# Optimization experiments

Measured on AMD Instinct MI355X. Metric: run time of the kernel, lower is better.

The kernel has to match this reference:

```python
import jax, jax.numpy as jnp
import numpy as np

D = 128        # embed_dims
P = 4          # num_points
G = 1          # num_groups
L = 4          # num_levels
NC = 6         # cameras
HB, WB = 200, 200
QN = HB * WB
NUM_LAYERS = 2
IMG_H, IMG_W = 256, 704
EPS = 1e-5
PC_MIN = np.array([-50.0, -50.0, -5.0], np.float32)
PC_EXT = np.array([100.0, 100.0, 8.0], np.float32)
LEVEL_HW = [(32, 88), (16, 44), (8, 22), (4, 11)]


def layer_norm(x, g, b):
    m = x.mean(-1, keepdims=True)
    v = jnp.mean((x - m) ** 2, axis=-1, keepdims=True)
    return (x - m) * jax.lax.rsqrt(v + 1e-5) * g + b


def bilinear(feat, u, v):
    # feat: (B,H,W,C); u,v: (B,N) normalized to [0,1]; zero padding, align_corners=False
    B, H, W, C = feat.shape
    x = u * W - 0.5
    y = v * H - 0.5
    x0f = jnp.floor(x)
    y0f = jnp.floor(y)
    wx = (x - x0f)[..., None]
    wy = (y - y0f)[..., None]
    x0 = x0f.astype(jnp.int32)
    y0 = y0f.astype(jnp.int32)
    bi = jnp.arange(B)[:, None]

    def gather(xi, yi):
        valid = ((xi >= 0) & (xi < W) & (yi >= 0) & (yi < H)).astype(feat.dtype)[..., None]
        return feat[bi, jnp.clip(yi, 0, H - 1), jnp.clip(xi, 0, W - 1)] * valid

    return (gather(x0, y0) * (1 - wx) * (1 - wy)
            + gather(x0 + 1, y0) * wx * (1 - wy)
            + gather(x0, y0 + 1) * (1 - wx) * wy
            + gather(x0 + 1, y0 + 1) * wx * wy)


def cam_contrib(l2i_n, hom, sw, cam_feats):
    # l2i_n: (B,4,4); hom: (B,Q,G,P,4); sw: (B,Q,G,P,L); cam_feats: L x (B,Hl,Wl,C)
    p2 = jnp.einsum('bij,bqgpj->bqgpi', l2i_n, hom)
    z = p2[..., 2]
    zc = jnp.maximum(z, EPS)
    u = p2[..., 0] / (zc * IMG_W)
    v = p2[..., 1] / (zc * IMG_H)
    mask = (z > EPS) & (u >= 0) & (u <= 1) & (v >= 0) & (v <= 1)
    B = hom.shape[0]
    uf = u.reshape(B, -1)
    vf = v.reshape(B, -1)
    out = jnp.zeros(hom.shape[:4] + (cam_feats[0].shape[-1],), cam_feats[0].dtype)
    for l in range(L):
        s = bilinear(cam_feats[l], uf, vf).reshape(B, -1, G, P, cam_feats[l].shape[-1])
        out = out + s * sw[..., l:l + 1]
    return out * mask[..., None].astype(out.dtype)


def forward(feat0, feat1, feat2, feat3, lidar2img, bev_query, bev_pos,
            pe_w1, pe_b1, pe_w2, pe_b2, conv1_w, conv1_b, conv2_w, conv2_b,
            off_w, off_b, sw_w, sw_b, cp_w1, cp_b1, cp_w2, cp_b2, cp_w3, cp_b3,
            ffn_w1, ffn_b1, ffn_w2, ffn_b2, n1_g, n1_b, n2_g, n2_b, n3_g, n3_b):
    # (b,n,C,h,w) -> (b,n,h,w,C), matching the decoder's rearrange (g=1)
    feats = [jnp.transpose(f, (0, 1, 3, 4, 2)) for f in (feat0, feat1, feat2, feat3)]
    B = bev_query.shape[0]
    pc_min = jnp.asarray(PC_MIN)
    pc_ext = jnp.asarray(PC_EXT)
    # position embedding of bev_pos is identical every layer
    pos_embed = jax.nn.relu(bev_pos @ pe_w1 + pe_b1) @ pe_w2 + pe_b2
    q = bev_query
    for _ in range(NUM_LAYERS):
        # in_conv: 1x1 conv + GELU + 5x5 conv on 200x200 BEV grid
        qe = (q + pos_embed).reshape(B, HB, WB, D)
        h = jax.nn.gelu(qe @ conv1_w + conv1_b, approximate=False)
        h = jax.lax.conv_general_dilated(h, conv2_w, (1, 1), 'SAME',
                                         dimension_numbers=('NHWC', 'HWIO', 'NHWC')) + conv2_b
        q = q + h.reshape(B, QN, D)
        q = layer_norm(q, n1_g, n1_b)
        # DetSegSampling
        off = (q @ off_w + off_b).reshape(B, QN, G, P, 3)
        ref = bev_pos[:, :, None, None, :] * pc_ext + pc_min
        pts = ref + off
        sw = jax.nn.softmax((q @ sw_w + sw_b).reshape(B, QN, G, P, L), axis=-1)
        hom = jnp.concatenate([pts, jnp.ones_like(pts[..., :1])], -1)
        acc = jnp.zeros((B, QN, G, P, D), q.dtype)
        for n in range(NC):
            acc = acc + cam_contrib(lidar2img[:, n], hom, sw,
                                    tuple(f[:, n] for f in feats))
        # 'b q g p c -> b q (p g c)' then 3-layer compressor MLP (1x1 convs)
        flat = jnp.transpose(acc, (0, 1, 3, 2, 4)).reshape(B, QN, P * G * D)
        h = jax.nn.relu(flat @ cp_w1 + cp_b1)
        h = jax.nn.relu(h @ cp_w2 + cp_b2)
        h = h @ cp_w3 + cp_b3
        q = q + h
        q = layer_norm(q, n2_g, n2_b)
        q = q + (jax.nn.relu(q @ ffn_w1 + ffn_b1) @ ffn_w2 + ffn_b2)
        q = layer_norm(q, n3_g, n3_b)
    return q


def _make_lidar2img():
    fx = fy = 500.0
    K = np.array([[fx, 0, IMG_W / 2, 0], [0, fy, IMG_H / 2, 0],
                  [0, 0, 1, 0], [0, 0, 0, 1]], np.float32)
    mats = []
    for n in range(NC):
        yaw = 2 * np.pi * n / NC
        c, s = np.cos(yaw), np.sin(yaw)
        # camera n looks along (cos yaw, sin yaw, 0), mounted 1.5m above lidar
        E = np.array([[s, -c, 0, 0], [0, 0, -1, 1.5], [c, s, 0, 0], [0, 0, 0, 1]], np.float32)
        mats.append(K @ E)
    return jnp.asarray(np.stack(mats))[None]  # (1,NC,4,4)


def setup_inputs() -> dict:
    key = jax.random.key(0)
    ks = jax.random.split(key, 24)
    sc = 0.02
    inp = {}
    for i, (h, w) in enumerate(LEVEL_HW):
        inp[f'feat{i}'] = jax.random.normal(ks[i], (1, NC, D, h, w), jnp.float32)
    inp['lidar2img'] = _make_lidar2img()
    inp['bev_query'] = jax.random.normal(ks[4], (1, QN, D), jnp.float32)
    inp['bev_pos'] = jax.random.uniform(ks[5], (1, QN, 3), jnp.float32)
    inp['pe_w1'] = jax.random.normal(ks[6], (3, 2 * D), jnp.float32) * sc
    inp['pe_b1'] = jnp.zeros((2 * D,), jnp.float32)
    inp['pe_w2'] = jax.random.normal(ks[7], (2 * D, D), jnp.float32) * sc
    inp['pe_b2'] = jnp.zeros((D,), jnp.float32)
    inp['conv1_w'] = jax.random.normal(ks[8], (D, D), jnp.float32) * sc
    inp['conv1_b'] = jnp.zeros((D,), jnp.float32)
    inp['conv2_w'] = jax.random.normal(ks[9], (5, 5, D, D), jnp.float32) * sc
    inp['conv2_b'] = jnp.zeros((D,), jnp.float32)
    inp['off_w'] = jax.random.normal(ks[10], (D, G * P * 3), jnp.float32) * 0.01
    inp['off_b'] = jax.random.uniform(ks[11], (G * P * 3,), jnp.float32, -0.5, 0.5)
    inp['sw_w'] = jax.random.normal(ks[12], (D, G * P * L), jnp.float32) * sc
    inp['sw_b'] = jnp.zeros((G * P * L,), jnp.float32)
    inp['cp_w1'] = jax.random.normal(ks[13], (P * G * D, 4 * D), jnp.float32) * sc
    inp['cp_b1'] = jnp.zeros((4 * D,), jnp.float32)
    inp['cp_w2'] = jax.random.normal(ks[14], (4 * D, 4 * D), jnp.float32) * sc
    inp['cp_b2'] = jnp.zeros((4 * D,), jnp.float32)
    inp['cp_w3'] = jax.random.normal(ks[15], (4 * D, D), jnp.float32) * sc
    inp['cp_b3'] = jnp.zeros((D,), jnp.float32)
    inp['ffn_w1'] = jax.random.normal(ks[16], (D, D), jnp.float32) * sc
    inp['ffn_b1'] = jnp.zeros((D,), jnp.float32)
    inp['ffn_w2'] = jax.random.normal(ks[17], (D, D), jnp.float32) * sc
    inp['ffn_b2'] = jnp.zeros((D,), jnp.float32)
    for i in (1, 2, 3):
        inp[f'n{i}_g'] = jnp.ones((D,), jnp.float32)
        inp[f'n{i}_b'] = jnp.zeros((D,), jnp.float32)
    return inp


def reference(feat0, feat1, feat2, feat3, lidar2img, bev_query, bev_pos,
              pe_w1, pe_b1, pe_w2, pe_b2, conv1_w, conv1_b, conv2_w, conv2_b,
              off_w, off_b, sw_w, sw_b, cp_w1, cp_b1, cp_w2, cp_b2, cp_w3, cp_b3,
              ffn_w1, ffn_b1, ffn_w2, ffn_b2, n1_g, n1_b, n2_g, n2_b, n3_g, n3_b):
    return forward(feat0, feat1, feat2, feat3, lidar2img, bev_query, bev_pos,
                   pe_w1, pe_b1, pe_w2, pe_b2, conv1_w, conv1_b, conv2_w, conv2_b,
                   off_w, off_b, sw_w, sw_b, cp_w1, cp_b1, cp_w2, cp_b2, cp_w3, cp_b3,
                   ffn_w1, ffn_b1, ffn_w2, ffn_b2, n1_g, n1_b, n2_g, n2_b, n3_g, n3_b)
```

## Files before the change

kernel.cpp:

```cpp
#include <hip/hip_runtime.h>
#include <hip/hip_bf16.h>

typedef unsigned short u16;
typedef unsigned char u8;
typedef __attribute__((ext_vector_type(8))) short bf16x8;
typedef __attribute__((ext_vector_type(4))) float f32x4;
typedef __attribute__((ext_vector_type(2))) float f32x2;

#define DEV __device__ __forceinline__

DEV float b2f(u16 s){ return __uint_as_float(((unsigned)s) << 16); }
DEV u16 f2b(float f){
    unsigned u = __float_as_uint(f);
    u = u + 0x7fffu + ((u >> 16) & 1u);
    return (u16)(u >> 16);
}
DEV u8 f2f8(float v){
    int r = __builtin_amdgcn_cvt_pk_fp8_f32(v, v, 0, false);
    return (u8)(r & 0xff);
}
DEV unsigned f2f8x4(float a, float b, float c, float d){
    int lo = __builtin_amdgcn_cvt_pk_fp8_f32(a, b, 0, false);
    int r  = __builtin_amdgcn_cvt_pk_fp8_f32(c, d, lo, true);
    return (unsigned)r;
}
DEV void storeElem(float* p, float v){ *p = v; }
DEV void storeElem(u16* p, float v){ *p = f2b(v); }
DEV void storeElem(u8* p, float v){ *p = f2f8(v); }

template<int ACT> DEV float actf(float x){
    if (ACT == 1) return fmaxf(x, 0.f);
    if (ACT == 2) return 0.5f * x * (1.f + erff(x * 0.70710678118654752f));
    return x;
}

DEV void gload16(const void* g, void* l){
    __builtin_amdgcn_global_load_lds(
        (const __attribute__((address_space(1))) void*)g,
        (__attribute__((address_space(3))) void*)l, 16, 0, 0);
}

__global__ void transpose_feat(const float* __restrict__ in, u8* __restrict__ out,
                               int H, int W){
    int total = 6 * H * W * 32;
    int lin = blockIdx.x * 256 + threadIdx.x;
    if (lin >= total) return;
    int c4   = (lin & 31) * 4;
    int pix  = lin >> 5;
    int x    = pix % W;
    int rest = pix / W;
    int y    = rest % H;
    int n    = rest / H;
    int HW   = H * W;
    size_t ib = ((size_t)(n * 128 + c4) * H + y) * W + x;
    unsigned v4 = f2f8x4(in[ib], in[ib + (size_t)HW],
                         in[ib + (size_t)2 * HW], in[ib + (size_t)3 * HW]);
    *(unsigned*)&out[(size_t)pix * 128 + c4] = v4;
}

__global__ void prep_wt(const float* __restrict__ w, u16* __restrict__ o, int K, int N){
    int id = blockIdx.x * 256 + threadIdx.x;
    if (id >= K * N) return;
    int n = id / K, k = id % K;
    o[id] = f2b(w[(size_t)k * N + n]);
}
__global__ void prep_wt_f8(const float* __restrict__ w, u8* __restrict__ o, int K, int N){
    int id = blockIdx.x * 256 + threadIdx.x;
    if (id >= K * N) return;
    int n = id / K, k = id % K;
    o[id] = f2f8(w[(size_t)k * N + n]);
}
__global__ void prep_cvt16(const float* __restrict__ src, u16* __restrict__ dst, int n4){
    int i4 = blockIdx.x * 256 + threadIdx.x;
    if (i4 >= n4) return;
    float4 a = *(const float4*)&src[(size_t)i4 * 4];
    ushort4 v; v.x = f2b(a.x); v.y = f2b(a.y); v.z = f2b(a.z); v.w = f2b(a.w);
    *(ushort4*)&dst[(size_t)i4 * 4] = v;
}
__global__ void prep_osw_w(const float* __restrict__ off_w, const float* __restrict__ off_b,
                           const float* __restrict__ sw_w, const float* __restrict__ sw_b,
                           u16* __restrict__ owsT, float* __restrict__ obias){
    int id = blockIdx.x * 256 + threadIdx.x;
    if (id >= 4096) return;
    int n = id >> 7, k = id & 127;
    float w = (n < 12) ? off_w[k * 12 + n] : (n < 28) ? sw_w[k * 16 + (n - 12)] : 0.f;
    owsT[n * 128 + k] = f2b(w);
    if (k == 0) obias[n] = (n < 12) ? off_b[n] : (n < 28) ? sw_b[n - 12] : 0.f;
}
__global__ void prep_conv_w_f8(const float* __restrict__ w, u8* __restrict__ o){
    int id = blockIdx.x * 256 + threadIdx.x;
    if (id >= 51200) return;
    int slot = id & 15;
    int oc   = (id >> 4) & 127;
    int tap  = id >> 11;
    int ks = slot >> 2, kg = slot & 3;
    int ic0 = ks * 32 + kg * 8;
    u8 tmp[8];
#pragma unroll
    for (int j = 0; j < 8; j++)
        tmp[j] = f2f8(w[((size_t)tap * 128 + ic0 + j) * 128 + oc]);
    *(long*)&o[(size_t)tap * 16384 + ks * 4096 + kg * 1024 + oc * 8] = *(long*)tmp;
}
__global__ void prep_hid(const float* __restrict__ bev_pos,
                         const float* __restrict__ w1, const float* __restrict__ b1,
                         u16* __restrict__ hid){
    int id = blockIdx.x * 256 + threadIdx.x;
    if (id >= 2560000) return;
    int qi = id >> 6, c4 = (id & 63) * 4;
    float p0 = bev_pos[qi * 3 + 0];
    float p1 = bev_pos[qi * 3 + 1];
    float p2 = bev_pos[qi * 3 + 2];
    ushort4 v;
    u16* vp = (u16*)&v;
#pragma unroll
    for (int j = 0; j < 4; j++){
        int ch = c4 + j;
        float h = p0 * w1[ch] + p1 * w1[256 + ch] + p2 * w1[512 + ch] + b1[ch];
        vp[j] = f2b(fmaxf(h, 0.f));
    }
    *(ushort4*)&hid[(size_t)qi * 256 + c4] = v;
}

DEV void stage64(const u16* __restrict__ g, int ldk, u16* lds, int wv, int lane){
    const u16* gp = g + (size_t)(lane >> 3) * ldk + (lane & 7) * 8;
#pragma unroll
    for (int j = 0; j < 4; j++){
        int ch = wv + j * 4;
        gload16(gp + (size_t)ch * 8 * ldk, lds + ch * 512);
    }
}
DEV void stage64f8(const u8* __restrict__ g, int ldk, u8* lds, int wv, int lane){
    int rloc = lane >> 2;
#pragma unroll
    for (int j = 0; j < 2; j++){
        int ch = wv + j * 4;
        int row = ch * 16 + rloc;
        int sp  = (lane & 3) ^ ((row >> 1) & 3);
        gload16(g + (size_t)row * ldk + sp * 16, lds + ch * 1024);
    }
}

template<int K, int ACT, typename TOUT, int NBY = 0, int NBX = 0>
__global__ __launch_bounds__(256) void mfma_gemm(
    const u16* __restrict__ A, const u16* __restrict__ BT,
    const float* __restrict__ bias, TOUT* __restrict__ C, int Ntot){
    __shared__ u16 As[2][128 * 64];
    __shared__ u16 Bs[2][128 * 64];
    const int t = threadIdx.x, wv = t >> 6, lane = t & 63;
    int bx, by;
    if (NBY > 0){
        const int gpx = (NBX + 7) / 8;
        int xcd = blockIdx.x & 7, slot = blockIdx.x >> 3;
        bx = xcd * gpx + slot / NBY;
        by = slot % NBY;
        if (bx >= NBX) return;
    } else { bx = blockIdx.x; by = blockIdx.y; }
    const int r0 = bx * 128, n0 = by * 128;
    const int l15 = lane & 15, kg = lane >> 4;
    const int wr = (wv >> 1) * 64, wc = (wv & 1) * 64;
    f32x4 acc[4][4];
#pragma unroll
    for (int r = 0; r < 4; r++)
#pragma unroll
        for (int c = 0; c < 4; c++) acc[r][c] = (f32x4){0.f, 0.f, 0.f, 0.f};

    stage64(A + (size_t)r0 * K, K, As[0], wv, lane);
    stage64(BT + (size_t)n0 * K, K, Bs[0], wv, lane);
    __syncthreads();
    int buf = 0;
    for (int kc = 0; kc < K / 64; kc++){
        if (kc + 1 < K / 64){
            stage64(A + (size_t)r0 * K + (kc + 1) * 64, K, As[buf ^ 1], wv, lane);
            stage64(BT + (size_t)n0 * K + (kc + 1) * 64, K, Bs[buf ^ 1], wv, lane);
        }
#pragma unroll
        for (int ks = 0; ks < 2; ks++){
            bf16x8 af[4], bfr[4];
#pragma unroll
            for (int r = 0; r < 4; r++)
                af[r] = *(const bf16x8*)&As[buf][(wr + r * 16 + l15) * 64 + ks * 32 + kg * 8];
#pragma unroll
            for (int c = 0; c < 4; c++)
                bfr[c] = *(const bf16x8*)&Bs[buf][(wc + c * 16 + l15) * 64 + ks * 32 + kg * 8];
#pragma unroll
            for (int r = 0; r < 4; r++)
#pragma unroll
                for (int c = 0; c < 4; c++)
                    acc[r][c] = __builtin_amdgcn_mfma_f32_16x16x32_bf16(af[r], bfr[c], acc[r][c], 0, 0, 0);
        }
        __syncthreads();
        buf ^= 1;
    }
#pragma unroll
    for (int c = 0; c < 4; c++){
        int gcol = n0 + wc + c * 16 + l15;
        float bb = bias[gcol];
#pragma unroll
        for (int r = 0; r < 4; r++){
#pragma unroll
            for (int reg = 0; reg < 4; reg++){
                int grow = r0 + wr + r * 16 + kg * 4 + reg;
                storeElem(C + (size_t)grow * Ntot + gcol, actf<ACT>(acc[r][c][reg] + bb));
            }
        }
    }
}

template<int K, int ACT, typename TOUT, int NBY = 0, int NBX = 0>
__global__ __launch_bounds__(256) void mfma_gemm_f8(
    const u8* __restrict__ A, const u8* __restrict__ BT,
    const float* __restrict__ bias, TOUT* __restrict__ C, int Ntot){
    __shared__ __align__(16) u8 As[2][128 * 64];
    __shared__ __align__(16) u8 Bs[2][128 * 64];
    const int t = threadIdx.x, wv = t >> 6, lane = t & 63;
    int bx, by;
    if (NBY > 0){
        const int gpx = (NBX + 7) / 8;
        int xcd = blockIdx.x & 7, slot = blockIdx.x >> 3;
        bx = xcd * gpx + slot / NBY;
        by = slot % NBY;
        if (bx >= NBX) return;
    } else { bx = blockIdx.x; by = blockIdx.y; }
    const int r0 = bx * 128, n0 = by * 128;
    const int l15 = lane & 15, kg = lane >> 4;
    const int wr = (wv >> 1) * 64, wc = (wv & 1) * 64;
    f32x4 acc[4][4];
#pragma unroll
    for (int r = 0; r < 4; r++)
#pragma unroll
        for (int c = 0; c < 4; c++) acc[r][c] = (f32x4){0.f, 0.f, 0.f, 0.f};

    stage64f8(A + (size_t)r0 * K, K, As[0], wv, lane);
    stage64f8(BT + (size_t)n0 * K, K, Bs[0], wv, lane);
    __syncthreads();
    int buf = 0;
    for (int kc = 0; kc < K / 64; kc++){
        if (kc + 1 < K / 64){
            stage64f8(A + (size_t)r0 * K + (kc + 1) * 64, K, As[buf ^ 1], wv, lane);
            stage64f8(BT + (size_t)n0 * K + (kc + 1) * 64, K, Bs[buf ^ 1], wv, lane);
        }
#pragma unroll
        for (int ks = 0; ks < 2; ks++){
            long af[4], bfr[4];
#pragma unroll
            for (int r = 0; r < 4; r++){
                int row = wr + r * 16 + l15;
                int s8 = (ks * 4 + kg) ^ (row & 6);
                af[r] = *(const long*)&As[buf][row * 64 + s8 * 8];
            }
#pragma unroll
            for (int c = 0; c < 4; c++){
                int row = wc + c * 16 + l15;
                int s8 = (ks * 4 + kg) ^ (row & 6);
                bfr[c] = *(const long*)&Bs[buf][row * 64 + s8 * 8];
            }
#pragma unroll
            for (int r = 0; r < 4; r++)
#pragma unroll
                for (int c = 0; c < 4; c++)
                    acc[r][c] = __builtin_amdgcn_mfma_f32_16x16x32_fp8_fp8(af[r], bfr[c], acc[r][c], 0, 0, 0);
        }
        __syncthreads();
        buf ^= 1;
    }
#pragma unroll
    for (int c = 0; c < 4; c++){
        int gcol = n0 + wc + c * 16 + l15;
        float bb = bias[gcol];
#pragma unroll
        for (int r = 0; r < 4; r++){
#pragma unroll
            for (int reg = 0; reg < 4; reg++){
                int grow = r0 + wr + r * 16 + kg * 4 + reg;
                storeElem(C + (size_t)grow * Ntot + gcol, actf<ACT>(acc[r][c][reg] + bb));
            }
        }
    }
}

__global__ __launch_bounds__(256) void mfma_pos(
    const u16* __restrict__ A, const u16* __restrict__ BT,
    const float* __restrict__ bias, const float* __restrict__ bq,
    float* __restrict__ pos, u16* __restrict__ qp16){
    const int K = 256;
    __shared__ u16 As[2][128 * 64];
    __shared__ u16 Bs[2][128 * 64];
    const int t = threadIdx.x, wv = t >> 6, lane = t & 63;
    const int r0 = blockIdx.x * 128;
    const int l15 = lane & 15, kg = lane >> 4;
    const int wr = (wv >> 1) * 64, wc = (wv & 1) * 64;
    f32x4 acc[4][4];
#pragma unroll
    for (int r = 0; r < 4; r++)
#pragma unroll
        for (int c = 0; c < 4; c++) acc[r][c] = (f32x4){0.f, 0.f, 0.f, 0.f};

    stage64(A + (size_t)r0 * K, K, As[0], wv, lane);
    stage64(BT, K, Bs[0], wv, lane);
    __syncthreads();
    int buf = 0;
    for (int kc = 0; kc < 4; kc++){
        if (kc + 1 < 4){
            stage64(A + (size_t)r0 * K + (kc + 1) * 64, K, As[buf ^ 1], wv, lane);
            stage64(BT + (kc + 1) * 64, K, Bs[buf ^ 1], wv, lane);
        }
#pragma unroll
        for (int ks = 0; ks < 2; ks++){
            bf16x8 af[4], bfr[4];
#pragma unroll
            for (int r = 0; r < 4; r++)
                af[r] = *(const bf16x8*)&As[buf][(wr + r * 16 + l15) * 64 + ks * 32 + kg * 8];
#pragma unroll
            for (int c = 0; c < 4; c++)
                bfr[c] = *(const bf16x8*)&Bs[buf][(wc + c * 16 + l15) * 64 + ks * 32 + kg * 8];
#pragma unroll
            for (int r = 0; r < 4; r++)
#pragma unroll
                for (int c = 0; c < 4; c++)
                    acc[r][c] = __builtin_amdgcn_mfma_f32_16x16x32_bf16(af[r], bfr[c], acc[r][c], 0, 0, 0);
        }
        __syncthreads();
        buf ^= 1;
    }
#pragma unroll
    for (int c = 0; c < 4; c++){
        int gcol = wc + c * 16 + l15;
        float bb = bias[gcol];
#pragma unroll
        for (int r = 0; r < 4; r++){
#pragma unroll
            for (int reg = 0; reg < 4; reg++){
                int grow = r0 + wr + r * 16 + kg * 4 + reg;
                int growc = min(grow, 39999);
                float v = acc[r][c][reg] + bb;
                pos[(size_t)grow * 128 + gcol]  = v;
                qp16[(size_t)grow * 128 + gcol] = f2b(v + bq[(size_t)growc * 128 + gcol]);
            }
        }
    }
}

template<int AUXM>
__global__ __launch_bounds__(256) void mfma_ffn_ln(
    const u16* __restrict__ A, const u16* __restrict__ W1T,
    const float* __restrict__ b1, const u16* __restrict__ W2T,
    const float* __restrict__ b2, const u16* __restrict__ qin16,
    const float* __restrict__ gam, const float* __restrict__ bet,
    float* __restrict__ outf, u16* __restrict__ q16out, u16* __restrict__ auxpos,
    const float* __restrict__ pos, int Mlim){
    __shared__ u16 As[2][128 * 64];
    __shared__ u16 Bs[2][128 * 64];
    const int t = threadIdx.x, wv = t >> 6, lane = t & 63;
    const int r0 = blockIdx.x * 128;
    const int l15 = lane & 15, kg = lane >> 4;
    const int wr = wv * 32;
    f32x4 acc[2][8];
#pragma unroll
    for (int r = 0; r < 2; r++)
#pragma unroll
        for (int c = 0; c < 8; c++) acc[r][c] = (f32x4){0.f, 0.f, 0.f, 0.f};

    stage64(A + (size_t)r0 * 128, 128, As[0], wv, lane);
    stage64(A + (size_t)r0 * 128 + 64, 128, As[1], wv, lane);
    stage64(W1T, 128, Bs[0], wv, lane);
    stage64(W1T + 64, 128, Bs[1], wv, lane);
    __syncthreads();
#pragma unroll
    for (int kc = 0; kc < 2; kc++){
#pragma unroll
        for (int ks = 0; ks < 2; ks++){
            bf16x8 af[2], bfr[8];
#pragma unroll
            for (int r = 0; r < 2; r++)
                af[r] = *(const bf16x8*)&As[kc][(wr + r * 16 + l15) * 64 + ks * 32 + kg * 8];
#pragma unroll
            for (int c = 0; c < 8; c++)
                bfr[c] = *(const bf16x8*)&Bs[kc][(c * 16 + l15) * 64 + ks * 32 + kg * 8];
#pragma unroll
            for (int r = 0; r < 2; r++)
#pragma unroll
                for (int c = 0; c < 8; c++)
                    acc[r][c] = __builtin_amdgcn_mfma_f32_16x16x32_bf16(af[r], bfr[c], acc[r][c], 0, 0, 0);
        }
    }
    __syncthreads();
    stage64(W2T, 128, Bs[0], wv, lane);
    stage64(W2T + 64, 128, Bs[1], wv, lane);
#pragma unroll
    for (int c = 0; c < 8; c++){
        int col = c * 16 + l15;
        float bb1 = b1[col];
#pragma unroll
        for (int r = 0; r < 2; r++)
#pragma unroll
            for (int reg = 0; reg < 4; reg++){
                int rowl = wr + r * 16 + kg * 4 + reg;
                As[col >> 6][rowl * 64 + (col & 63)] = f2b(fmaxf(acc[r][c][reg] + bb1, 0.f));
            }
    }
    __syncthreads();
#pragma unroll
    for (int r = 0; r < 2; r++)
#pragma unroll
        for (int c = 0; c < 8; c++) acc[r][c] = (f32x4){0.f, 0.f, 0.f, 0.f};
#pragma unroll
    for (int kc = 0; kc < 2; kc++){
#pragma unroll
        for (int ks = 0; ks < 2; ks++){
            bf16x8 af[2], bfr[8];
#pragma unroll
            for (int r = 0; r < 2; r++)
                af[r] = *(const bf16x8*)&As[kc][(wr + r * 16 + l15) * 64 + ks * 32 + kg * 8];
#pragma unroll
            for (int c = 0; c < 8; c++)
                bfr[c] = *(const bf16x8*)&Bs[kc][(c * 16 + l15) * 64 + ks * 32 + kg * 8];
#pragma unroll
            for (int r = 0; r < 2; r++)
#pragma unroll
                for (int c = 0; c < 8; c++)
                    acc[r][c] = __builtin_amdgcn_mfma_f32_16x16x32_bf16(af[r], bfr[c], acc[r][c], 0, 0, 0);
        }
    }
    float bb[8], gg[8], be[8];
#pragma unroll
    for (int c = 0; c < 8; c++){
        int col = c * 16 + l15;
        bb[c] = b2[col]; gg[c] = gam[col]; be[c] = bet[col];
    }
#pragma unroll
    for (int r = 0; r < 2; r++){
#pragma unroll
        for (int reg = 0; reg < 4; reg++){
            int grow = r0 + wr + r * 16 + kg * 4 + reg;
            const u16* qrow = qin16 + (size_t)grow * 128;
            float s = 0.f, q2 = 0.f;
#pragma unroll
            for (int c = 0; c < 8; c++){
                float x = acc[r][c][reg] + bb[c] + b2f(qrow[c * 16 + l15]);
                acc[r][c][reg] = x;
                s += x; q2 += x * x;
            }
#pragma unroll
            for (int m = 8; m >= 1; m >>= 1){
                s  += __shfl_xor(s, m, 64);
                q2 += __shfl_xor(q2, m, 64);
            }
            float mean = s * 0.0078125f;
            float var  = q2 * 0.0078125f - mean * mean;
            float rs   = rsqrtf(var + 1e-5f);
            bool wr_ok = grow < Mlim;
#pragma unroll
            for (int c = 0; c < 8; c++){
                float o = (acc[r][c][reg] - mean) * rs * gg[c] + be[c];
                int col = c * 16 + l15;
                if (wr_ok){
                    if (AUXM == 0){
                        outf[(size_t)grow * 128 + col] = o;
                    } else {
                        q16out[(size_t)grow * 128 + col] = f2b(o);
                        auxpos[(size_t)grow * 128 + col] = f2b(o + pos[(size_t)grow * 128 + col]);
                    }
                }
            }
        }
    }
}

template<int K>
__global__ __launch_bounds__(256) void mfma_gemm_ln_f8(
    const u8* __restrict__ A, const u8* __restrict__ BT,
    const float* __restrict__ bias, const u16* __restrict__ qin16,
    const float* __restrict__ gam, const float* __restrict__ bet,
    u16* __restrict__ q16out, int Mlim){
    __shared__ __align__(16) u8 As[2][128 * 64];
    __shared__ __align__(16) u8 Bs[2][128 * 64];
    const int t = threadIdx.x, wv = t >> 6, lane = t & 63;
    const int r0 = blockIdx.x * 128;
    const int l15 = lane & 15, kg = lane >> 4;
    const int wr = wv * 32;
    f32x4 acc[2][8];
#pragma unroll
    for (int r = 0; r < 2; r++)
#pragma unroll
        for (int c = 0; c < 8; c++) acc[r][c] = (f32x4){0.f, 0.f, 0.f, 0.f};

    stage64f8(A + (size_t)r0 * K, K, As[0], wv, lane);
    stage64f8(BT, K, Bs[0], wv, lane);
    __syncthreads();
    int buf = 0;
    for (int kc = 0; kc < K / 64; kc++){
        if (kc + 1 < K / 64){
            stage64f8(A + (size_t)r0 * K + (kc + 1) * 64, K, As[buf ^ 1], wv, lane);
            stage64f8(BT + (kc + 1) * 64, K, Bs[buf ^ 1], wv, lane);
        }
#pragma unroll
        for (int ks = 0; ks < 2; ks++){
            long af[2], bfr[8];
#pragma unroll
            for (int r = 0; r < 2; r++){
                int row = wr + r * 16 + l15;
                int s8 = (ks * 4 + kg) ^ (row & 6);
                af[r] = *(const long*)&As[buf][row * 64 + s8 * 8];
            }
#pragma unroll
            for (int c = 0; c < 8; c++){
                int row = c * 16 + l15;
                int s8 = (ks * 4 + kg) ^ (row & 6);
                bfr[c] = *(const long*)&Bs[buf][row * 64 + s8 * 8];
            }
#pragma unroll
            for (int r = 0; r < 2; r++)
#pragma unroll
                for (int c = 0; c < 8; c++)
                    acc[r][c] = __builtin_amdgcn_mfma_f32_16x16x32_fp8_fp8(af[r], bfr[c], acc[r][c], 0, 0, 0);
        }
        __syncthreads();
        buf ^= 1;
    }
    float bb[8], gg[8], be[8];
#pragma unroll
    for (int c = 0; c < 8; c++){
        int col = c * 16 + l15;
        bb[c] = bias[col]; gg[c] = gam[col]; be[c] = bet[col];
    }
#pragma unroll
    for (int r = 0; r < 2; r++){
#pragma unroll
        for (int reg = 0; reg < 4; reg++){
            int grow = r0 + wr + r * 16 + kg * 4 + reg;
            const u16* qrow = qin16 + (size_t)grow * 128;
            float s = 0.f, q2 = 0.f;
#pragma unroll
            for (int c = 0; c < 8; c++){
                float x = acc[r][c][reg] + bb[c] + b2f(qrow[c * 16 + l15]);
                acc[r][c][reg] = x;
                s += x; q2 += x * x;
            }
#pragma unroll
            for (int m = 8; m >= 1; m >>= 1){
                s  += __shfl_xor(s, m, 64);
                q2 += __shfl_xor(q2, m, 64);
            }
            float mean = s * 0.0078125f;
            float var  = q2 * 0.0078125f - mean * mean;
            float rs   = rsqrtf(var + 1e-5f);
            bool wr_ok = grow < Mlim;
#pragma unroll
            for (int c = 0; c < 8; c++){
                float o = (acc[r][c][reg] - mean) * rs * gg[c] + be[c];
                if (wr_ok) q16out[(size_t)grow * 128 + c * 16 + l15] = f2b(o);
            }
        }
    }
}

__global__ __launch_bounds__(256) void mfma_osw(
    const u16* __restrict__ A, const u16* __restrict__ BT,
    const float* __restrict__ bias, float* __restrict__ osw){
    __shared__ u16 As[2][128 * 64];
    __shared__ u16 Bs[2][32 * 64];
    const int t = threadIdx.x, wv = t >> 6, lane = t & 63;
    const int r0 = blockIdx.x * 128;
    const int l15 = lane & 15, kg = lane >> 4;
#pragma unroll
    for (int it = 0; it < 8; it++){
        int id = it * 256 + t;
        int row = id >> 4, slot = id & 15;
        uint4 v = *(const uint4*)&A[(size_t)(r0 + row) * 128 + slot * 8];
        *(uint4*)&As[slot >> 3][row * 64 + (slot & 7) * 8] = v;
    }
#pragma unroll
    for (int it = 0; it < 2; it++){
        int id = it * 256 + t;
        if (id < 512){
            int row = id >> 4, slot = id & 15;
            uint4 v = *(const uint4*)&BT[(size_t)row * 128 + slot * 8];
            *(uint4*)&Bs[slot >> 3][row * 64 + (slot & 7) * 8] = v;
        }
    }
    __syncthreads();
    f32x4 acc[2][2];
#pragma unroll
    for (int r = 0; r < 2; r++)
#pragma unroll
        for (int c = 0; c < 2; c++) acc[r][c] = (f32x4){0.f, 0.f, 0.f, 0.f};
#pragma unroll
    for (int ks = 0; ks < 4; ks++){
        int h = ks >> 1, koff = (ks & 1) * 32 + kg * 8;
        bf16x8 af[2], bfr[2];
#pragma unroll
        for (int r = 0; r < 2; r++)
            af[r] = *(const bf16x8*)&As[h][(wv * 32 + r * 16 + l15) * 64 + koff];
#pragma unroll
        for (int c = 0; c < 2; c++)
            bfr[c] = *(const bf16x8*)&Bs[h][(c * 16 + l15) * 64 + koff];
#pragma unroll
        for (int r = 0; r < 2; r++)
#pragma unroll
            for (int c = 0; c < 2; c++)
                acc[r][c] = __builtin_amdgcn_mfma_f32_16x16x32_bf16(af[r], bfr[c], acc[r][c], 0, 0, 0);
    }
#pragma unroll
    for (int c = 0; c < 2; c++){
        int gcol = c * 16 + l15;
        float bb = bias[gcol];
#pragma unroll
        for (int r = 0; r < 2; r++)
#pragma unroll
            for (int reg = 0; reg < 4; reg++){
                int grow = r0 + wv * 32 + r * 16 + kg * 4 + reg;
                osw[(size_t)grow * 32 + gcol] = acc[r][c][reg] + bb;
            }
    }
}

__global__ __launch_bounds__(256) void proj_kernel(
    const float* __restrict__ osw, const float* __restrict__ bev_pos,
    const float* __restrict__ l2i, uint4* __restrict__ ent4, int* __restrict__ cntb){
    int id = blockIdx.x * 256 + threadIdx.x;
    int qi = id >> 2, p = id & 3;
    const float* row = osw + (size_t)qi * 32;
    float px = bev_pos[qi * 3 + 0] * 100.f - 50.f + row[p * 3 + 0];
    float py = bev_pos[qi * 3 + 1] * 100.f - 50.f + row[p * 3 + 1];
    float pz = bev_pos[qi * 3 + 2] * 8.f   - 5.f  + row[p * 3 + 2];
    float lg[4];
#pragma unroll
    for (int l = 0; l < 4; l++) lg[l] = row[12 + p * 4 + l];
    float mx = fmaxf(fmaxf(lg[0], lg[1]), fmaxf(lg[2], lg[3]));
    float den = 0.f, sw[4];
#pragma unroll
    for (int l = 0; l < 4; l++){ sw[l] = expf(lg[l] - mx); den += sw[l]; }
    float inv = 1.f / den;
#pragma unroll
    for (int l = 0; l < 4; l++) sw[l] *= inv;

    const int HS[4] = {32, 16, 8, 4};
    const int WS[4] = {88, 44, 22, 11};
    const unsigned LOFF[4] = {0u, 2162688u, 2703360u, 2838528u};
    int cnt = 0;
    for (int cam = 0; cam < 6; cam++){
        const float* M = l2i + cam * 16;
        float t0 = M[0] * px + M[1] * py + M[2]  * pz + M[3];
        float t1 = M[4] * px + M[5] * py + M[6]  * pz + M[7];
        float z  = M[8] * px + M[9] * py + M[10] * pz + M[11];
        float zc = fmaxf(z, 1e-5f);
        float u = t0 / (zc * 704.f);
        float v = t1 / (zc * 256.f);
        if (!((z > 1e-5f) && u >= 0.f && u <= 1.f && v >= 0.f && v <= 1.f)) continue;
#pragma unroll
        for (int l = 0; l < 4; l++){
            const int Hl = HS[l], Wl = WS[l];
            float xx = u * (float)Wl - 0.5f;
            float yy = v * (float)Hl - 0.5f;
            float xf = floorf(xx), yf = floorf(yy);
            float wx = xx - xf, wy = yy - yf;
            int ix = (int)xf, iy = (int)yf;
            float sl = sw[l];
            float wx0 = (ix >= 0)      ? 1.f - wx : 0.f;
            float wx1 = (ix < Wl - 1)  ? wx       : 0.f;
            float wy0 = (iy >= 0)      ? 1.f - wy : 0.f;
            float wy1 = (iy < Hl - 1)  ? wy       : 0.f;
            int x0c = max(ix, 0), x1c = min(ix + 1, Wl - 1);
            int y0c = max(iy, 0), y1c = min(iy + 1, Hl - 1);
            unsigned base = LOFF[l] + (unsigned)cam * (unsigned)(Hl * Wl * 128)
                          + (unsigned)(y0c * Wl + x0c) * 128u;
            unsigned dxdy = (unsigned)((x1c - x0c) * 128)
                          | ((unsigned)((y1c - y0c) * Wl * 128) << 16);
            if (cnt < 8){
                uint4 e4;
                e4.x = (unsigned)f2b(sl * wx0 * wy0) | ((unsigned)f2b(sl * wx1 * wy0) << 16);
                e4.y = (unsigned)f2b(sl * wx0 * wy1) | ((unsigned)f2b(sl * wx1 * wy1) << 16);
                e4.z = base;
                e4.w = dxdy;
                ent4[(size_t)cnt * 160000 + id] = e4;
                cnt++;
            }
        }
    }
    cntb[id] = cnt;
}

DEV void fma8f8(float* acc, uint2 v, float w){
    f32x2 p0 = __builtin_amdgcn_cvt_pk_f32_fp8(v.x, false);
    f32x2 p1 = __builtin_amdgcn_cvt_pk_f32_fp8(v.x, true);
    f32x2 p2 = __builtin_amdgcn_cvt_pk_f32_fp8(v.y, false);
    f32x2 p3 = __builtin_amdgcn_cvt_pk_f32_fp8(v.y, true);
    acc[0] = fmaf(p0.x, w, acc[0]);
    acc[1] = fmaf(p0.y, w, acc[1]);
    acc[2] = fmaf(p1.x, w, acc[2]);
    acc[3] = fmaf(p1.y, w, acc[3]);
    acc[4] = fmaf(p2.x, w, acc[4]);
    acc[5] = fmaf(p2.y, w, acc[5]);
    acc[6] = fmaf(p3.x, w, acc[6]);
    acc[7] = fmaf(p3.y, w, acc[7]);
}

__global__ __launch_bounds__(256) void sample_kernel(
    const uint4* __restrict__ ent4, const int* __restrict__ cntb,
    const u8* __restrict__ ftbase, u8* __restrict__ flat){
    const int t = threadIdx.x;
    const int lane = t & 15;
    const int id = blockIdx.x * 16 + (t >> 4);
    const int d0 = lane * 8;
    const int cnt = cntb[id];
    float acc[8] = {0, 0, 0, 0, 0, 0, 0, 0};

    uint4 evA, evB;
    if (cnt > 0) evA = ent4[(size_t)id];
    for (int e = 0; e < cnt; e++){
        if (e + 1 < cnt) evB = ent4[(size_t)(e + 1) * 160000 + id];
        unsigned base = evA.z + (unsigned)d0;
        unsigned dx = evA.w & 0xffffu, dy = evA.w >> 16;
        uint2 v00 = *(const uint2*)(ftbase + base);
        uint2 v10 = *(const uint2*)(ftbase + base + dx);
        uint2 v01 = *(const uint2*)(ftbase + base + dy);
        uint2 v11 = *(const uint2*)(ftbase + base + dx + dy);
        fma8f8(acc, v00, b2f((u16)(evA.x & 0xffffu)));
        fma8f8(acc, v10, b2f((u16)(evA.x >> 16)));
        fma8f8(acc, v01, b2f((u16)(evA.y & 0xffffu)));
        fma8f8(acc, v11, b2f((u16)(evA.y >> 16)));
        evA = evB;
    }
    uint2 o;
    o.x = f2f8x4(acc[0], acc[1], acc[2], acc[3]);
    o.y = f2f8x4(acc[4], acc[5], acc[6], acc[7]);
    *(uint2*)&flat[(size_t)id * 128 + d0] = o;
}

#define ALOAD(S, DST) if ((S) < 100){                                                 \
    const int tap_ = (S) >> 2, ks_ = (S) & 3;                                         \
    const int ky_ = tap_ / 5, kx_ = tap_ - ky_ * 5;                                   \
    const int s8_ = ks_ * 4 + kg;                                                     \
    _Pragma("unroll")                                                                 \
    for (int fb = 0; fb < 2; fb++){                                                   \
        _Pragma("unroll")                                                             \
        for (int fp = 0; fp < 2; fp++){                                               \
            int pr_ = fb * 4 + (l15 >> 2) + ky_;                                      \
            int pc_ = fp * 4 + (l15 & 3) + kx_;                                       \
            int pix_ = pr_ * 12 + pc_;                                                \
            int sw_ = ((s8_ >> 1) ^ (pc_ + 4 * pr_)) & 7;                             \
            DST[fb * 2 + fp] = *(const long*)((const char*)Ps + pix_ * 128            \
                                              + sw_ * 16 + (s8_ & 1) * 8);            \
        }                                                                             \
    }                                                                                 \
}
#define CMFMA(CURA, CURB) {                                                           \
    _Pragma("unroll")                                                                 \
    for (int fr = 0; fr < 4; fr++){                                                   \
        acc[fr][0] = __builtin_amdgcn_mfma_f32_16x16x32_fp8_fp8(CURA[fr], CURB[0], acc[fr][0], 0, 0, 0); \
        acc[fr][1] = __builtin_amdgcn_mfma_f32_16x16x32_fp8_fp8(CURA[fr], CURB[1], acc[fr][1], 0, 0, 0); \
    }                                                                                 \
}
#define LOADB(S, DST) if ((S) < 100){                                                 \
    const u8* wp_ = wfrag + ((S) >> 2) * 16384 + ((S) & 3) * 4096                     \
                   + kg * 1024 + (wc + l15) * 8;                                      \
    DST[0] = *(const long*)(wp_);                                                     \
    DST[1] = *(const long*)(wp_ + 128);                                               \
}

__global__ __launch_bounds__(256, 4) void conv5_ln(
    const u8* __restrict__ in,
    const u8* __restrict__ wfrag,
    const float* __restrict__ bias,
    const u16* __restrict__ qin16,
    const float* __restrict__ gam, const float* __restrict__ bet,
    u16* __restrict__ q16){
    __shared__ __align__(16) u8 Ps[144 * 128];
    const int t = threadIdx.x, wv = t >> 6, lane = t & 63;
    const int bx = blockIdx.x % 25, by = blockIdx.x / 25;
    const int x0 = bx * 8, y0 = by * 8;
    const int l15 = lane & 15, kg = lane >> 4;
    const int wc = wv * 32;

#pragma unroll
    for (int it = 0; it < 5; it++){
        int id = it * 256 + t;
        if (id < 1152){
            int pix = id >> 3, slot = id & 7;
            int pr = pix / 12, pc = pix - pr * 12;
            int gy = y0 + pr - 2, gx = x0 + pc - 2;
            uint4 v = {0u, 0u, 0u, 0u};
            if (gy >= 0 && gy < 200 && gx >= 0 && gx < 200)
                v = *(const uint4*)&in[(size_t)(gy * 200 + gx) * 128 + slot * 16];
            int s = (slot ^ (pc + 4 * pr)) & 7;
            *(uint4*)((char*)Ps + pix * 128 + s * 16) = v;
        }
    }
    f32x4 acc[4][2];
#pragma unroll
    for (int r = 0; r < 4; r++){
        acc[r][0] = (f32x4){0.f, 0.f, 0.f, 0.f};
        acc[r][1] = (f32x4){0.f, 0.f, 0.f, 0.f};
    }

    long b0[2], b1[2], b2[2], b3[2];
    LOADB(0, b0); LOADB(1, b1); LOADB(2, b2);
    __syncthreads();

    long aA[4], aB[4];
    ALOAD(0, aA);

    for (int i = 0; i < 25; i++){
        int s = i * 4;
        LOADB(s + 3, b3); ALOAD(s + 1, aB); CMFMA(aA, b0);
        LOADB(s + 4, b0); ALOAD(s + 2, aA); CMFMA(aB, b1);
        LOADB(s + 5, b1); ALOAD(s + 3, aB); CMFMA(aA, b2);
        LOADB(s + 6, b2); ALOAD(s + 4, aA); CMFMA(aB, b3);
    }
    __syncthreads();

    float* part = (float*)Ps;
    float bb[2], gg[2], be[2];
#pragma unroll
    for (int c = 0; c < 2; c++){
        int oc = wc + c * 16 + l15;
        bb[c] = bias[oc]; gg[c] = gam[oc]; be[c] = bet[oc];
    }
#pragma unroll
    for (int fb = 0; fb < 2; fb++){
#pragma unroll
        for (int fp = 0; fp < 2; fp++){
#pragma unroll
            for (int reg = 0; reg < 4; reg++){
                int py = fb * 4 + kg, px = fp * 4 + reg;
                int lp = py * 8 + px;
                int grow = (y0 + py) * 200 + x0 + px;
                const u16* qrow = qin16 + (size_t)grow * 128;
                float s = 0.f, q2 = 0.f;
#pragma unroll
                for (int c = 0; c < 2; c++){
                    float x = acc[fb * 2 + fp][c][reg] + bb[c] + b2f(qrow[wc + c * 16 + l15]);
                    acc[fb * 2 + fp][c][reg] = x;
                    s += x; q2 += x * x;
                }
#pragma unroll
                for (int msk = 8; msk >= 1; msk >>= 1){
                    s  += __shfl_xor(s, msk, 64);
                    q2 += __shfl_xor(q2, msk, 64);
                }
                if (l15 == 0){
                    part[lp * 8 + wv * 2 + 0] = s;
                    part[lp * 8 + wv * 2 + 1] = q2;
                }
            }
        }
    }
    __syncthreads();
#pragma unroll
    for (int fb = 0; fb < 2; fb++){
#pragma unroll
        for (int fp = 0; fp < 2; fp++){
#pragma unroll
            for (int reg = 0; reg < 4; reg++){
                int py = fb * 4 + kg, px = fp * 4 + reg;
                int lp = py * 8 + px;
                int grow = (y0 + py) * 200 + x0 + px;
                float s  = part[lp * 8 + 0] + part[lp * 8 + 2] + part[lp * 8 + 4] + part[lp * 8 + 6];
                float q2 = part[lp * 8 + 1] + part[lp * 8 + 3] + part[lp * 8 + 5] + part[lp * 8 + 7];
                float mean = s * 0.0078125f;
                float var  = q2 * 0.0078125f - mean * mean;
                float rs   = rsqrtf(var + 1e-5f);
#pragma unroll
                for (int c = 0; c < 2; c++){
                    int oc = wc + c * 16 + l15;
                    float o = (acc[fb * 2 + fp][c][reg] - mean) * rs * gg[c] + be[c];
                    q16[(size_t)grow * 128 + oc] = f2b(o);
                }
            }
        }
    }
}

extern "C" void kernel_launch(void* const* d_in, const int* in_sizes, int n_in,
                              void* d_out, int out_size, void* d_ws, size_t ws_size,
                              hipStream_t stream){
    const float* feat0   = (const float*)d_in[0];
    const float* feat1   = (const float*)d_in[1];
    const float* feat2   = (const float*)d_in[2];
    const float* feat3   = (const float*)d_in[3];
    const float* l2i     = (const float*)d_in[4];
    const float* bev_q   = (const float*)d_in[5];
    const float* bev_pos = (const float*)d_in[6];
    const float* pe_w1   = (const float*)d_in[7];
    const float* pe_b1   = (const float*)d_in[8];
    const float* pe_w2   = (const float*)d_in[9];
    const float* pe_b2   = (const float*)d_in[10];
    const float* conv1_w = (const float*)d_in[11];
    const float* conv1_b = (const float*)d_in[12];
    const float* conv2_w = (const float*)d_in[13];
    const float* conv2_b = (const float*)d_in[14];
    const float* off_w   = (const float*)d_in[15];
    const float* off_b   = (const float*)d_in[16];
    const float* sw_w    = (const float*)d_in[17];
    const float* sw_b    = (const float*)d_in[18];
    const float* cp_w1   = (const float*)d_in[19];
    const float* cp_b1   = (const float*)d_in[20];
    const float* cp_w2   = (const float*)d_in[21];
    const float* cp_b2   = (const float*)d_in[22];
    const float* cp_w3   = (const float*)d_in[23];
    const float* cp_b3   = (const float*)d_in[24];
    const float* ffn_w1  = (const float*)d_in[25];
    const float* ffn_b1  = (const float*)d_in[26];
    const float* ffn_w2  = (const float*)d_in[27];
    const float* ffn_b2  = (const float*)d_in[28];
    const float* n1g = (const float*)d_in[29];
    const float* n1b = (const float*)d_in[30];
    const float* n2g = (const float*)d_in[31];
    const float* n2b = (const float*)d_in[32];
    const float* n3g = (const float*)d_in[33];
    const float* n3b = (const float*)d_in[34];

    float* base   = (float*)d_ws;
    float* pos    = base;
    u16*   bq16   = (u16*)(base + 5128192);
    float* hbuf   = base + 10256384;
    u8*    h18    = (u8*)hbuf;
    uint4* ent4   = (uint4*)hbuf;
    u16*   q16    = (u16*)(base + 20512768);
    u16*   qpos16 = (u16*)(base + 23076864);
    int*   cntb   = (int*)qpos16;
    u8*    bufA8  = (u8*)(base + 25640960);
    float* osw    = (float*)(base + 25640960 + 1310720);
    u8*    flat8  = (u8*)(base + 28205056);
    u16*   hid16  = (u16*)flat8;
    u8*    ft0    = (u8*)(base + 38461440);
    u8*    ft1    = ft0 + 6 * 32 * 88 * 128;
    u8*    ft2    = ft1 + 6 * 16 * 44 * 128;
    u8*    ft3    = ft2 + 6 * 8 * 22 * 128;
    u8*    w1t8   = (u8*)(base + 39897600);
    u8*    w2t8   = w1t8 + 512 * 512;
    u8*    w3t8   = w2t8 + 512 * 512;
    u16*   wc1t   = (u16*)(base + 40192512);
    u16*   wf1t   = (u16*)(base + 40200704);
    u16*   wf2t   = (u16*)(base + 40208896);
    u16*   owsT   = (u16*)(base + 40217088);
    float* obias  = (float*)(base + 40219136);
    u8*    wcs8   = (u8*)(base + 40219168);
    u16*   pw2t   = (u16*)(base + 40424168);
    float* outp   = (float*)d_out;

    transpose_feat<<<(6 * 32 * 88 * 32 + 255) / 256, 256, 0, stream>>>(feat0, ft0, 32, 88);
    transpose_feat<<<(6 * 16 * 44 * 32 + 255) / 256, 256, 0, stream>>>(feat1, ft1, 16, 44);
    transpose_feat<<<(6 * 8 * 22 * 32 + 255) / 256, 256, 0, stream>>>(feat2, ft2, 8, 22);
    transpose_feat<<<(6 * 4 * 11 * 32 + 255) / 256, 256, 0, stream>>>(feat3, ft3, 4, 11);
    prep_wt_f8<<<(512 * 512 + 255) / 256, 256, 0, stream>>>(cp_w1, w1t8, 512, 512);
    prep_wt_f8<<<(512 * 512 + 255) / 256, 256, 0, stream>>>(cp_w2, w2t8, 512, 512);
    prep_wt_f8<<<(512 * 128 + 255) / 256, 256, 0, stream>>>(cp_w3, w3t8, 512, 128);
    prep_wt<<<(128 * 128 + 255) / 256, 256, 0, stream>>>(conv1_w, wc1t, 128, 128);
    prep_wt<<<(128 * 128 + 255) / 256, 256, 0, stream>>>(ffn_w1, wf1t, 128, 128);
    prep_wt<<<(128 * 128 + 255) / 256, 256, 0, stream>>>(ffn_w2, wf2t, 128, 128);
    prep_wt<<<(256 * 128 + 255) / 256, 256, 0, stream>>>(pe_w2, pw2t, 256, 128);
    prep_osw_w<<<16, 256, 0, stream>>>(off_w, off_b, sw_w, sw_b, owsT, obias);
    prep_conv_w_f8<<<(51200 + 255) / 256, 256, 0, stream>>>(conv2_w, wcs8);
    prep_cvt16<<<5000, 256, 0, stream>>>(bev_q, bq16, 1280000);
    prep_hid<<<10000, 256, 0, stream>>>(bev_pos, pe_w1, pe_b1, hid16);
    mfma_pos<<<313, 256, 0, stream>>>(hid16, pw2t, pe_b2, bev_q, pos, qpos16);

    for (int layer = 0; layer < 2; layer++){
        const u16* qin16 = layer ? q16 : bq16;
        mfma_gemm<128, 2, u8><<<dim3(313, 1), 256, 0, stream>>>(qpos16, wc1t, conv1_b, bufA8, 128);
        conv5_ln<<<625, 256, 0, stream>>>(bufA8, wcs8, conv2_b, qin16, n1g, n1b, q16);
        mfma_osw<<<313, 256, 0, stream>>>(q16, owsT, obias, osw);
        proj_kernel<<<625, 256, 0, stream>>>(osw, bev_pos, l2i, ent4, cntb);
        sample_kernel<<<10000, 256, 0, stream>>>(ent4, cntb, ft0, flat8);
        mfma_gemm_f8<512, 1, u8, 4, 313><<<1280, 256, 0, stream>>>(flat8, w1t8, cp_b1, h18, 512);
        mfma_gemm_f8<512, 1, u8, 4, 313><<<1280, 256, 0, stream>>>(h18, w2t8, cp_b2, flat8, 512);
        mfma_gemm_ln_f8<512><<<313, 256, 0, stream>>>(flat8, w3t8, cp_b3, q16, n2g, n2b,
                                                      q16, 40064);
        if (layer == 0)
            mfma_ffn_ln<2><<<313, 256, 0, stream>>>(q16, wf1t, ffn_b1, wf2t, ffn_b2,
                                                    q16, n3g, n3b, nullptr, q16, qpos16, pos, 40064);
        else
            mfma_ffn_ln<0><<<313, 256, 0, stream>>>(q16, wf1t, ffn_b1, wf2t, ffn_b2,
                                                    q16, n3g, n3b, outp, nullptr, nullptr, nullptr, 40000);
    }
}
```

Before: 422.6 us.

## Fuse positional-encoding hidden layer into pos GEMM and pad conv LDS rows

Removes the separate prep_hid kernel and instead computes the ReLU(bev_pos*W1+b1) hidden activations directly into LDS inside mfma_pos for each K chunk. This avoids writing and re-reading a 40000x256 bf16 intermediate through global memory, at the cost of recomputing small dot products per tile. Separately, the conv5_ln staging tile switches from an XOR-swizzled 128-byte row layout to a padded 136-byte row layout to avoid bank conflicts with simpler addressing. The padded layout needs split 8-byte stores and slightly more LDS.

```diff
diff --git a/kernel.cpp b/kernel.cpp
--- a/kernel.cpp
+++ b/kernel.cpp
@@ -100,25 +100,6 @@
     for (int j = 0; j < 8; j++)
         tmp[j] = f2f8(w[((size_t)tap * 128 + ic0 + j) * 128 + oc]);
     *(long*)&o[(size_t)tap * 16384 + ks * 4096 + kg * 1024 + oc * 8] = *(long*)tmp;
-}
-__global__ void prep_hid(const float* __restrict__ bev_pos,
-                         const float* __restrict__ w1, const float* __restrict__ b1,
-                         u16* __restrict__ hid){
-    int id = blockIdx.x * 256 + threadIdx.x;
-    if (id >= 2560000) return;
-    int qi = id >> 6, c4 = (id & 63) * 4;
-    float p0 = bev_pos[qi * 3 + 0];
-    float p1 = bev_pos[qi * 3 + 1];
-    float p2 = bev_pos[qi * 3 + 2];
-    ushort4 v;
-    u16* vp = (u16*)&v;
-#pragma unroll
-    for (int j = 0; j < 4; j++){
-        int ch = c4 + j;
-        float h = p0 * w1[ch] + p1 * w1[256 + ch] + p2 * w1[512 + ch] + b1[ch];
-        vp[j] = f2b(fmaxf(h, 0.f));
-    }
-    *(ushort4*)&hid[(size_t)qi * 256 + c4] = v;
 }
 
 DEV void stage64(const u16* __restrict__ g, int ldk, u16* lds, int wv, int lane){
@@ -279,10 +260,11 @@
 }
 
 __global__ __launch_bounds__(256) void mfma_pos(
-    const u16* __restrict__ A, const u16* __restrict__ BT,
-    const float* __restrict__ bias, const float* __restrict__ bq,
+    const float* __restrict__ bev_pos,
+    const float* __restrict__ w1, const float* __restrict__ b1,
+    const u16* __restrict__ BT, const float* __restrict__ bias,
+    const float* __restrict__ bq,
     float* __restrict__ pos, u16* __restrict__ qp16){
-    const int K = 256;
     __shared__ u16 As[2][128 * 64];
     __shared__ u16 Bs[2][128 * 64];
     const int t = threadIdx.x, wv = t >> 6, lane = t & 63;
@@ -295,14 +277,35 @@
 #pragma unroll
         for (int c = 0; c < 4; c++) acc[r][c] = (f32x4){0.f, 0.f, 0.f, 0.f};
 
-    stage64(A + (size_t)r0 * K, K, As[0], wv, lane);
-    stage64(BT, K, Bs[0], wv, lane);
+    auto hidchunk = [&](int kc, u16* dst){
+#pragma unroll
+        for (int i = 0; i < 4; i++){
+            int task = i * 256 + t;
+            int row = task >> 3, k8 = (task & 7) * 8;
+            int grow = min(r0 + row, 39999);
+            float p0 = bev_pos[grow * 3 + 0];
+            float p1 = bev_pos[grow * 3 + 1];
+            float p2 = bev_pos[grow * 3 + 2];
+            int ch0 = kc * 64 + k8;
+            u16 tmp[8];
+#pragma unroll
+            for (int j = 0; j < 8; j++){
+                int ch = ch0 + j;
+                float h = p0 * w1[ch] + p1 * w1[256 + ch] + p2 * w1[512 + ch] + b1[ch];
+                tmp[j] = f2b(fmaxf(h, 0.f));
+            }
+            *(uint4*)&dst[row * 64 + k8] = *(uint4*)tmp;
+        }
+    };
+
+    hidchunk(0, As[0]);
+    stage64(BT, 256, Bs[0], wv, lane);
     __syncthreads();
     int buf = 0;
     for (int kc = 0; kc < 4; kc++){
         if (kc + 1 < 4){
-            stage64(A + (size_t)r0 * K + (kc + 1) * 64, K, As[buf ^ 1], wv, lane);
-            stage64(BT + (kc + 1) * 64, K, Bs[buf ^ 1], wv, lane);
+            stage64(BT + (kc + 1) * 64, 256, Bs[buf ^ 1], wv, lane);
+            hidchunk(kc + 1, As[buf ^ 1]);
         }
 #pragma unroll
         for (int ks = 0; ks < 2; ks++){
@@ -738,9 +741,7 @@
             int pr_ = fb * 4 + (l15 >> 2) + ky_;                                      \
             int pc_ = fp * 4 + (l15 & 3) + kx_;                                       \
             int pix_ = pr_ * 12 + pc_;                                                \
-            int sw_ = ((s8_ >> 1) ^ (pc_ + 4 * pr_)) & 7;                             \
-            DST[fb * 2 + fp] = *(const long*)((const char*)Ps + pix_ * 128            \
-                                              + sw_ * 16 + (s8_ & 1) * 8);            \
+            DST[fb * 2 + fp] = *(const long*)((const char*)Ps + pix_ * 136 + s8_ * 8);\
         }                                                                             \
     }                                                                                 \
 }
@@ -765,7 +766,7 @@
     const u16* __restrict__ qin16,
     const float* __restrict__ gam, const float* __restrict__ bet,
     u16* __restrict__ q16){
-    __shared__ __align__(16) u8 Ps[144 * 128];
+    __shared__ __align__(16) u8 Ps[144 * 136];
     const int t = threadIdx.x, wv = t >> 6, lane = t & 63;
     const int bx = blockIdx.x % 25, by = blockIdx.x / 25;
     const int x0 = bx * 8, y0 = by * 8;
@@ -782,8 +783,11 @@
             uint4 v = {0u, 0u, 0u, 0u};
             if (gy >= 0 && gy < 200 && gx >= 0 && gx < 200)
                 v = *(const uint4*)&in[(size_t)(gy * 200 + gx) * 128 + slot * 16];
-            int s = (slot ^ (pc + 4 * pr)) & 7;
-            *(uint4*)((char*)Ps + pix * 128 + s * 16) = v;
+            char* dst = (char*)Ps + pix * 136 + slot * 16;
+            uint2 lo; lo.x = v.x; lo.y = v.y;
+            uint2 hi; hi.x = v.z; hi.y = v.w;
+            *(uint2*)dst = lo;
+            *(uint2*)(dst + 8) = hi;
         }
     }
     f32x4 acc[4][2];
@@ -922,7 +926,6 @@
     u8*    bufA8  = (u8*)(base + 25640960);
     float* osw    = (float*)(base + 25640960 + 1310720);
     u8*    flat8  = (u8*)(base + 28205056);
-    u16*   hid16  = (u16*)flat8;
     u8*    ft0    = (u8*)(base + 38461440);
     u8*    ft1    = ft0 + 6 * 32 * 88 * 128;
     u8*    ft2    = ft1 + 6 * 16 * 44 * 128;
@@ -953,8 +956,7 @@
     prep_osw_w<<<16, 256, 0, stream>>>(off_w, off_b, sw_w, sw_b, owsT, obias);
     prep_conv_w_f8<<<(51200 + 255) / 256, 256, 0, stream>>>(conv2_w, wcs8);
     prep_cvt16<<<5000, 256, 0, stream>>>(bev_q, bq16, 1280000);
-    prep_hid<<<10000, 256, 0, stream>>>(bev_pos, pe_w1, pe_b1, hid16);
-    mfma_pos<<<313, 256, 0, stream>>>(hid16, pw2t, pe_b2, bev_q, pos, qpos16);
+    mfma_pos<<<313, 256, 0, stream>>>(bev_pos, pe_w1, pe_b1, pw2t, pe_b2, bev_q, pos, qpos16);
 
     for (int layer = 0; layer < 2; layer++){
         const u16* qin16 = layer ? q16 : bq16;
```

Measured after the change: 440.8 us. +4.3%, slower.
